# Kernel optimization log

Hardware: AMD Instinct MI355X
Metric: run time of the kernel (lower is better)

The kernel has to match this reference:

```python
import jax, jax.numpy as jnp
import numpy as np

NUM_HEADS = 32
HEAD_DIM = 128
NUM_KV_HEADS = 8
SCALE = 0.08838834764831845  # 1/sqrt(128)
T = 2048          # total packed tokens (total_q == total_k in delta branch)
N_SAL = 512       # number of salient rows
NUM_SEQS = 4
EPS = 1e-8
NEG = -1e30


def setup_inputs() -> dict:
    key = jax.random.key(0)
    ks = jax.random.split(key, 5)
    q = jax.random.normal(ks[0], (T, NUM_HEADS, HEAD_DIM), dtype=jnp.float32)
    k = jax.random.normal(ks[1], (T, NUM_KV_HEADS, HEAD_DIM), dtype=jnp.float32)
    v = jax.random.normal(ks[2], (N_SAL, NUM_KV_HEADS, HEAD_DIM), dtype=jnp.float32)
    v_cache = jax.random.normal(ks[3], (T, NUM_KV_HEADS, HEAD_DIM), dtype=jnp.float32)
    c_cache = jax.random.normal(ks[4], (T, NUM_HEADS * HEAD_DIM), dtype=jnp.float32)
    # unique, sorted salient row indices (torch index_copy requires well-defined scatter)
    idx_salient_row = (jnp.arange(N_SAL, dtype=jnp.int64) * (T // N_SAL))
    # 4 equal packed sequences
    cu_seqlens = jnp.array([0, 512, 1024, 1536, 2048], dtype=jnp.int64)
    return {"q": q, "k": k, "v": v, "v_cache": v_cache, "c_cache": c_cache,
            "idx_salient_row": idx_salient_row, "cu_seqlens": cu_seqlens}


def _segment_ids(cu_seqlens, n):
    # seg[i] = which packed sequence row i belongs to (searchsorted right on bounds)
    return jnp.searchsorted(cu_seqlens[1:], jnp.arange(n), side="right")


def _sdpa(q_, k_, v_, seg_q_, seg_k_):
    # GQA: repeat_interleave kv heads to match query heads
    n_rep = q_.shape[1] // k_.shape[1]
    if n_rep > 1:
        k_ = jnp.repeat(k_, n_rep, axis=1)
        v_ = jnp.repeat(v_, n_rep, axis=1)
    scores = jnp.einsum("qhd,khd->hqk", q_, k_) * SCALE  # [H, nq, T]
    allow = (seg_q_[:, None] == seg_k_[None, :])          # [nq, T]
    scores = jnp.where(allow[None, :, :], scores, NEG)
    p = jax.nn.softmax(scores, axis=-1)
    return jnp.einsum("hqk,khd->qhd", p, v_)              # [nq, H, D]


def reference(q, k, v, v_cache, c_cache, idx_salient_row, cu_seqlens):
    total = q.shape[0]
    seg = _segment_ids(cu_seqlens, total)  # seg_q == seg_k (total_q == total_k)

    # delta KV-cache update at salient rows
    v_delta = v - v_cache[idx_salient_row]                      # [n_sal, Hkv, D]
    v_delta_sparse = jnp.zeros_like(k).at[idx_salient_row].set(v_delta)
    v_cache_new = v_cache.at[idx_salient_row].set(v)

    # salient-row full attention against updated cache
    o_salient = _sdpa(q[idx_salient_row], k, v_cache_new, seg[idx_salient_row], seg)
    # sparse delta attention for every row
    delta_c = _sdpa(q, k, v_delta_sparse, seg, seg)

    new_c_flat = c_cache + delta_c.reshape(total, -1)
    new_c_flat = new_c_flat.at[idx_salient_row].set(o_salient.reshape(o_salient.shape[0], -1))

    # cosine similarity between old and new context (early-exit signal)
    num = jnp.sum(c_cache * new_c_flat, axis=-1)
    den_c = jnp.sum(c_cache * c_cache, axis=-1)
    den_n = jnp.sum(new_c_flat * new_c_flat, axis=-1)
    cos_sim = num / (jnp.sqrt(den_c) * jnp.sqrt(den_n) + EPS)

    return new_c_flat.reshape(total, NUM_HEADS, HEAD_DIM), cos_sim
```

## Files before the change

kernel.cpp:

```cpp
#include <hip/hip_runtime.h>
#include <math.h>

#define NUM_HEADS 32
#define HEAD_DIM 128
#define NUM_KV_HEADS 8
#define SCALE 0.08838834764831845f
#define EPS 1e-8f
#define MAX_SEG 512
#define QT 32
#define BLK 512
#define SEGC_MAX 16
#define PD_CHUNKS 4
#define SAL_PAD 576
#define PB_STRIDE 520
#define PD_STRIDE 136
#define TLD 130
#define CD (NUM_HEADS * HEAD_DIM)

typedef __bf16 bf16x8 __attribute__((ext_vector_type(8)));
typedef __bf16 bf16x4 __attribute__((ext_vector_type(4)));
typedef float  f32x4  __attribute__((ext_vector_type(4)));

__device__ __forceinline__ int lower_bound_i(const int* __restrict__ a, int n, int key) {
    int lo = 0, hi = n;
    while (lo < hi) { int mid = (lo + hi) >> 1; if (a[mid] < key) lo = mid + 1; else hi = mid; }
    return lo;
}
__device__ __forceinline__ int bsearch_eq(const int* __restrict__ a, int n, int key) {
    int lo = lower_bound_i(a, n, key);
    return (lo < n && a[lo] == key) ? lo : -1;
}

__global__ void prep(const float* __restrict__ k, const float* __restrict__ v,
                     const float* __restrict__ vc, const int* __restrict__ idx,
                     __bf16* __restrict__ kb, __bf16* __restrict__ vnewT,
                     __bf16* __restrict__ vdT, int T, int Tpad, int n_sal,
                     int nb_conv, int nb_vt) {
    __shared__ __bf16 tile[64 * TLD];
    __shared__ int sal_of[64];
    const int b = blockIdx.x;
    const int tid = threadIdx.x;

    if (b < nb_conv) {
        int i = b * 256 + tid;
        int n8 = T * NUM_KV_HEADS * HEAD_DIM / 8;
        if (i < n8) {
            const float4* s4 = (const float4*)(k + (size_t)i * 8);
            float4 a = s4[0], bb = s4[1];
            bf16x8 o;
            o[0]=(__bf16)a.x; o[1]=(__bf16)a.y; o[2]=(__bf16)a.z; o[3]=(__bf16)a.w;
            o[4]=(__bf16)bb.x; o[5]=(__bf16)bb.y; o[6]=(__bf16)bb.z; o[7]=(__bf16)bb.w;
            *(bf16x8*)(kb + (size_t)i * 8) = o;
        }
        return;
    }
    if (b < nb_conv + nb_vt * NUM_KV_HEADS) {
        const int bb = b - nb_conv;
        const int kv = bb / nb_vt;
        const int r0 = (bb % nb_vt) * 64;
        if (tid < 64) sal_of[tid] = bsearch_eq(idx, n_sal, r0 + tid);
        __syncthreads();
        for (int ii = tid; ii < 64 * 32; ii += 256) {
            int r = ii >> 5, c4 = ii & 31;
            int row = r0 + r;
            float4 f = {0.f, 0.f, 0.f, 0.f};
            if (row < T) {
                int s2 = sal_of[r];
                const float* src = (s2 >= 0)
                    ? v  + ((size_t)s2  * NUM_KV_HEADS + kv) * HEAD_DIM
                    : vc + ((size_t)row * NUM_KV_HEADS + kv) * HEAD_DIM;
                f = *(const float4*)(src + c4 * 4);
            }
            __bf16* tp = &tile[r * TLD + c4 * 4];
            tp[0] = (__bf16)f.x; tp[1] = (__bf16)f.y; tp[2] = (__bf16)f.z; tp[3] = (__bf16)f.w;
        }
        __syncthreads();
        for (int ii = tid; ii < 128 * 8; ii += 256) {
            int d = ii >> 3, rg = ii & 7;
            int row_out = r0 + rg * 8;
            if (row_out < Tpad) {
                bf16x8 o;
#pragma unroll
                for (int j = 0; j < 8; j++) o[j] = tile[(rg * 8 + j) * TLD + d];
                *(bf16x8*)(vnewT + ((size_t)kv * HEAD_DIM + d) * Tpad + row_out) = o;
            }
        }
        return;
    }
    {
        const int bb = b - nb_conv - nb_vt * NUM_KV_HEADS;
        const int nvd = SAL_PAD / 64;
        const int kv = bb / nvd;
        const int s0 = (bb % nvd) * 64;
        for (int ii = tid; ii < 64 * 32; ii += 256) {
            int r = ii >> 5, c4 = ii & 31;
            int s = s0 + r;
            float4 f = {0.f, 0.f, 0.f, 0.f};
            if (s < n_sal) {
                int row = idx[s];
                float4 a = *(const float4*)(v  + ((size_t)s   * NUM_KV_HEADS + kv) * HEAD_DIM + c4 * 4);
                float4 bb2 = *(const float4*)(vc + ((size_t)row * NUM_KV_HEADS + kv) * HEAD_DIM + c4 * 4);
                f.x = a.x - bb2.x; f.y = a.y - bb2.y; f.z = a.z - bb2.z; f.w = a.w - bb2.w;
            }
            __bf16* tp = &tile[r * TLD + c4 * 4];
            tp[0] = (__bf16)f.x; tp[1] = (__bf16)f.y; tp[2] = (__bf16)f.z; tp[3] = (__bf16)f.w;
        }
        __syncthreads();
        for (int ii = tid; ii < 128 * 8; ii += 256) {
            int d = ii >> 3, rg = ii & 7;
            bf16x8 o;
#pragma unroll
            for (int j = 0; j < 8; j++) o[j] = tile[(rg * 8 + j) * TLD + d];
            *(bf16x8*)(vdT + ((size_t)kv * HEAD_DIM + d) * SAL_PAD + s0 + rg * 8) = o;
        }
    }
}

__global__ __launch_bounds__(BLK, 4)
void attn_mfma(const float* __restrict__ q, const __bf16* __restrict__ kb,
               const __bf16* __restrict__ vnewT, const __bf16* __restrict__ vdT,
               const float* __restrict__ c_cache, const int* __restrict__ cu,
               const int* __restrict__ idx, float* __restrict__ out_c,
               float* __restrict__ cospart, int T, int Tpad, int n_seq, int n_sal) {
    const int qt    = blockIdx.x;
    const int h     = blockIdx.y;
    const int kvh   = h >> 2;
    const int qrow0 = qt * QT;
    const int tid   = threadIdx.x;
    const int wave  = tid >> 6;
    const int lane  = tid & 63;
    const int lm    = lane & 15;
    const int quad  = lane >> 4;

    __shared__ __align__(16) __bf16 Pb[QT * PB_STRIDE];
    __shared__ __align__(16) __bf16 Pd[QT * PD_STRIDE];
    __shared__ int   scol[MAX_SEG];
    __shared__ float wred[8 * QT];
    __shared__ float linv[QT];
    __shared__ int   salrow[QT];

    int seg_start = 0, seg_end = T;
    for (int s = 0; s < n_seq; s++) {
        int a = cu[s], bnd = cu[s + 1];
        if (qrow0 >= a && qrow0 < bnd) { seg_start = a; seg_end = bnd; }
    }
    const int seg_len = seg_end - seg_start;
    const int s_lo = lower_bound_i(idx, n_sal, seg_start);
    const int s_hi = lower_bound_i(idx, n_sal, seg_end);
    const int nss  = s_hi - s_lo;
    const int ntiles = (seg_len + 15) >> 4;
    const int SEGC   = (seg_len + 31) >> 5;

    const int dim = wave * 16 + lm;

    const float* cbase = c_cache + (size_t)qrow0 * CD + h * HEAD_DIM + dim;
    float cold[2][4];
#pragma unroll
    for (int rt = 0; rt < 2; rt++)
#pragma unroll
        for (int r = 0; r < 4; r++)
            cold[rt][r] = cbase[(size_t)(rt * 16 + quad * 4 + r) * CD];

    if (tid < QT) salrow[tid] = bsearch_eq(idx, n_sal, qrow0 + tid);
    for (int s = tid; s < nss; s += BLK) scol[s] = idx[s_lo + s] - seg_start;
    if (ntiles * 16 < SEGC * 32) {
        for (int ii = tid; ii < QT * 16; ii += BLK) {
            int row = ii >> 4, col = ntiles * 16 + (ii & 15);
            Pb[row * PB_STRIDE + col] = (__bf16)0.f;
        }
    }

    bf16x8 aq[2][4];
#pragma unroll
    for (int rt = 0; rt < 2; rt++) {
        const float* qp = q + ((size_t)(qrow0 + rt * 16 + lm) * NUM_HEADS + h) * HEAD_DIM + quad * 8;
#pragma unroll
        for (int cc = 0; cc < 4; cc++) {
            float4 f0 = *(const float4*)(qp + cc * 32);
            float4 f1 = *(const float4*)(qp + cc * 32 + 4);
            bf16x8 a;
            a[0]=(__bf16)f0.x; a[1]=(__bf16)f0.y; a[2]=(__bf16)f0.z; a[3]=(__bf16)f0.w;
            a[4]=(__bf16)f1.x; a[5]=(__bf16)f1.y; a[6]=(__bf16)f1.z; a[7]=(__bf16)f1.w;
            aq[rt][cc] = a;
        }
    }

    float ps[2] = {0.f, 0.f};
#pragma unroll
    for (int tt = 0; tt < 4; tt++) {
        const int t = wave * 4 + tt;
        if (t < ntiles) {
            int key = seg_start + t * 16 + lm;
            if (key >= seg_start + seg_len) key = seg_start + seg_len - 1;
            const __bf16* kp = kb + ((size_t)key * NUM_KV_HEADS + kvh) * HEAD_DIM + quad * 8;
            bf16x8 bk[4];
#pragma unroll
            for (int cc = 0; cc < 4; cc++) bk[cc] = *(const bf16x8*)(kp + cc * 32);
            f32x4 acc[2] = {{0.f,0.f,0.f,0.f},{0.f,0.f,0.f,0.f}};
#pragma unroll
            for (int cc = 0; cc < 4; cc++) {
                acc[0] = __builtin_amdgcn_mfma_f32_16x16x32_bf16(bk[cc], aq[0][cc], acc[0], 0, 0, 0);
                acc[1] = __builtin_amdgcn_mfma_f32_16x16x32_bf16(bk[cc], aq[1][cc], acc[1], 0, 0, 0);
            }
#pragma unroll
            for (int rt = 0; rt < 2; rt++) {
                bf16x4 pk;
#pragma unroll
                for (int r = 0; r < 4; r++) {
                    const int kl = t * 16 + quad * 4 + r;
                    float e = (kl < seg_len) ? __expf(acc[rt][r] * SCALE) : 0.f;
                    ps[rt] += e;
                    pk[r] = (__bf16)e;
                }
                *(bf16x4*)&Pb[(rt * 16 + lm) * PB_STRIDE + t * 16 + quad * 4] = pk;
            }
        }
    }
#pragma unroll
    for (int m = 16; m <= 32; m <<= 1) {
        ps[0] += __shfl_xor(ps[0], m, 64);
        ps[1] += __shfl_xor(ps[1], m, 64);
    }
    if (quad == 0) {
        wred[wave * QT + lm]      = ps[0];
        wred[wave * QT + 16 + lm] = ps[1];
    }
    __syncthreads();
    if (tid < QT) {
        float s = 0.f;
#pragma unroll
        for (int w = 0; w < 8; w++) s += wred[w * QT + tid];
        linv[tid] = 1.f / s;
    }

    f32x4 acc0a = {0.f,0.f,0.f,0.f}, acc0b = {0.f,0.f,0.f,0.f};
    f32x4 acc1a = {0.f,0.f,0.f,0.f}, acc1b = {0.f,0.f,0.f,0.f};
    const __bf16* vbase = vnewT + ((size_t)kvh * HEAD_DIM + dim) * Tpad + seg_start + quad * 8;
    const __bf16* pb0 = &Pb[lm * PB_STRIDE + quad * 8];
    const __bf16* pb1 = &Pb[(16 + lm) * PB_STRIDE + quad * 8];

#define PV_BODY(cc)  {                                                              \
        bf16x8 a0 = *(const bf16x8*)(pb0 + (cc) * 32);                              \
        bf16x8 a1 = *(const bf16x8*)(pb1 + (cc) * 32);                              \
        bf16x8 bv = *(const bf16x8*)(vbase + (cc) * 32);                            \
        if ((cc) & 1) {                                                             \
            acc0b = __builtin_amdgcn_mfma_f32_16x16x32_bf16(a0, bv, acc0b, 0, 0, 0);\
            acc1b = __builtin_amdgcn_mfma_f32_16x16x32_bf16(a1, bv, acc1b, 0, 0, 0);\
        } else {                                                                    \
            acc0a = __builtin_amdgcn_mfma_f32_16x16x32_bf16(a0, bv, acc0a, 0, 0, 0);\
            acc1a = __builtin_amdgcn_mfma_f32_16x16x32_bf16(a1, bv, acc1a, 0, 0, 0);\
        } }

    if (SEGC == SEGC_MAX) {
#pragma unroll
        for (int cc = 0; cc < SEGC_MAX; cc++) PV_BODY(cc)
    } else {
        for (int cc = 0; cc < SEGC; cc++) PV_BODY(cc)
    }
    f32x4 accF[2];
    accF[0] = acc0a + acc0b;
    accF[1] = acc1a + acc1b;

    f32x4 accD[2] = {{0.f,0.f,0.f,0.f},{0.f,0.f,0.f,0.f}};
    const int ndc = (nss + 31) >> 5;
    const bool al8 = ((s_lo & 7) == 0);
    const __bf16* vdbase = vdT + ((size_t)kvh * HEAD_DIM + dim) * SAL_PAD + s_lo + quad * 8;
    for (int base = 0; base < ndc; base += PD_CHUNKS) {
        const int bc = min(PD_CHUNKS, ndc - base);
        __syncthreads();
        for (int ii = tid; ii < QT * PD_CHUNKS * 32; ii += BLK) {
            int row = ii >> 7, srel = ii & 127;
            int s = base * 32 + srel;
            __bf16 e = (__bf16)0.f;
            if (srel < bc * 32 && s < nss) e = Pb[row * PB_STRIDE + scol[s]];
            Pd[row * PD_STRIDE + srel] = e;
        }
        __syncthreads();
#pragma unroll
        for (int dc = 0; dc < PD_CHUNKS; dc++) {
            if (dc < bc) {
                bf16x8 a0 = *(const bf16x8*)&Pd[lm * PD_STRIDE + dc * 32 + quad * 8];
                bf16x8 a1 = *(const bf16x8*)&Pd[(16 + lm) * PD_STRIDE + dc * 32 + quad * 8];
                const __bf16* vp = vdbase + (base + dc) * 32;
                bf16x8 bv;
                if (al8) bv = *(const bf16x8*)vp;
                else {
#pragma unroll
                    for (int j = 0; j < 8; j++) bv[j] = vp[j];
                }
                accD[0] = __builtin_amdgcn_mfma_f32_16x16x32_bf16(a0, bv, accD[0], 0, 0, 0);
                accD[1] = __builtin_amdgcn_mfma_f32_16x16x32_bf16(a1, bv, accD[1], 0, 0, 0);
            }
        }
    }
    __syncthreads();

    float* cp = (float*)Pd;
    float* obase = out_c + (size_t)qrow0 * CD + h * HEAD_DIM + dim;
#pragma unroll
    for (int rt = 0; rt < 2; rt++) {
#pragma unroll
        for (int r = 0; r < 4; r++) {
            const int row = rt * 16 + quad * 4 + r;
            const float c_old = cold[rt][r];
            const float li = linv[row];
            float o;
            if (salrow[row] >= 0) o = accF[rt][r] * li;
            else                  o = c_old + accD[rt][r] * li;
            obase[(size_t)row * CD] = o;
            float xn = o * c_old, xc = c_old * c_old, xd = o * o;
#pragma unroll
            for (int m = 1; m <= 8; m <<= 1) {
                xn += __shfl_xor(xn, m, 64);
                xc += __shfl_xor(xc, m, 64);
                xd += __shfl_xor(xd, m, 64);
            }
            if (lm == 0) {
                cp[(wave * 3 + 0) * QT + row] = xn;
                cp[(wave * 3 + 1) * QT + row] = xc;
                cp[(wave * 3 + 2) * QT + row] = xd;
            }
        }
    }
    __syncthreads();
    for (int ii = tid; ii < 3 * QT; ii += BLK) {
        int c = ii >> 5, row = ii & 31;
        float s = 0.f;
#pragma unroll
        for (int w = 0; w < 8; w++) s += cp[(w * 3 + c) * QT + row];
        cospart[((size_t)(qrow0 + row) * NUM_HEADS + h) * 3 + c] = s;
    }
}

__global__ void cos_finalize(const float* __restrict__ cospart, float* __restrict__ out_cos, int T) {
    int i = blockIdx.x * blockDim.x + threadIdx.x;
    if (i < T) {
        const float* p = cospart + (size_t)i * NUM_HEADS * 3;
        float n = 0.f, c = 0.f, d = 0.f;
#pragma unroll
        for (int h2 = 0; h2 < NUM_HEADS; h2++) {
            n += p[h2 * 3 + 0]; c += p[h2 * 3 + 1]; d += p[h2 * 3 + 2];
        }
        out_cos[i] = n / (sqrtf(c) * sqrtf(d) + EPS);
    }
}

extern "C" void kernel_launch(void* const* d_in, const int* in_sizes, int n_in,
                              void* d_out, int out_size, void* d_ws, size_t ws_size,
                              hipStream_t stream) {
    const float* q       = (const float*)d_in[0];
    const float* k       = (const float*)d_in[1];
    const float* v       = (const float*)d_in[2];
    const float* v_cache = (const float*)d_in[3];
    const float* c_cache = (const float*)d_in[4];
    const int*   idx     = (const int*)d_in[5];
    const int*   cu      = (const int*)d_in[6];

    const int T     = in_sizes[0] / CD;
    const int n_sal = in_sizes[5];
    const int n_seq = in_sizes[6] - 1;
    const int Tpad  = T + 32;

    float* out_c   = (float*)d_out;
    float* out_cos = out_c + (size_t)T * CD;

    char* wsp = (char*)d_ws;
    size_t off = 0;
    __bf16* kb = (__bf16*)(wsp + off);
    off += (((size_t)T * NUM_KV_HEADS * HEAD_DIM * 2) + 255) & ~(size_t)255;
    __bf16* vnewT = (__bf16*)(wsp + off);
    off += (((size_t)NUM_KV_HEADS * HEAD_DIM * Tpad * 2) + 255) & ~(size_t)255;
    __bf16* vdT = (__bf16*)(wsp + off);
    off += ((size_t)NUM_KV_HEADS * HEAD_DIM * SAL_PAD * 2 + 255) & ~(size_t)255;
    float* cospart = (float*)(wsp + off);
    off += ((size_t)T * NUM_HEADS * 3 * 4 + 255) & ~(size_t)255;
    (void)ws_size;

    const int nb_conv = (T * NUM_KV_HEADS * HEAD_DIM / 8 + 255) / 256;
    const int nb_vt   = (Tpad + 63) / 64;
    const int nb_vd   = SAL_PAD / 64;
    const int nb_tot  = nb_conv + nb_vt * NUM_KV_HEADS + nb_vd * NUM_KV_HEADS;

    prep<<<nb_tot, 256, 0, stream>>>(k, v, v_cache, idx, kb, vnewT, vdT,
                                     T, Tpad, n_sal, nb_conv, nb_vt);

    dim3 grid(T / QT, NUM_HEADS);
    attn_mfma<<<grid, BLK, 0, stream>>>(q, kb, vnewT, vdT, c_cache, cu, idx,
                                        out_c, cospart, T, Tpad, n_seq, n_sal);

    cos_finalize<<<(T + 255) / 256, 256, 0, stream>>>(cospart, out_cos, T);
}
```

Measured before the change: 240.9 us.

## Prefetch K, V and delta-V into registers and merge PV with delta MFMA loop

```diff
diff --git a/kernel.cpp b/kernel.cpp
--- a/kernel.cpp
+++ b/kernel.cpp
@@ -150,16 +150,15 @@
     const int nss  = s_hi - s_lo;
     const int ntiles = (seg_len + 15) >> 4;
     const int SEGC   = (seg_len + 31) >> 5;
+    const int ndc    = (nss + 31) >> 5;
+    const bool al8   = ((s_lo & 7) == 0);
+    const bool fast  = (SEGC == SEGC_MAX) && (ndc <= PD_CHUNKS);
 
     const int dim = wave * 16 + lm;
-
-    const float* cbase = c_cache + (size_t)qrow0 * CD + h * HEAD_DIM + dim;
-    float cold[2][4];
-#pragma unroll
-    for (int rt = 0; rt < 2; rt++)
-#pragma unroll
-        for (int r = 0; r < 4; r++)
-            cold[rt][r] = cbase[(size_t)(rt * 16 + quad * 4 + r) * CD];
+    const __bf16* vbase  = vnewT + ((size_t)kvh * HEAD_DIM + dim) * Tpad + seg_start + quad * 8;
+    const __bf16* vdbase = vdT + ((size_t)kvh * HEAD_DIM + dim) * SAL_PAD + s_lo + quad * 8;
+    const __bf16* pb0 = &Pb[lm * PB_STRIDE + quad * 8];
+    const __bf16* pb1 = &Pb[(16 + lm) * PB_STRIDE + quad * 8];
 
     if (tid < QT) salrow[tid] = bsearch_eq(idx, n_sal, qrow0 + tid);
     for (int s = tid; s < nss; s += BLK) scol[s] = idx[s_lo + s] - seg_start;
@@ -185,7 +184,7 @@
         }
     }
 
-    float ps[2] = {0.f, 0.f};
+    bf16x8 bk[4][4];
 #pragma unroll
     for (int tt = 0; tt < 4; tt++) {
         const int t = wave * 4 + tt;
@@ -193,14 +192,21 @@
             int key = seg_start + t * 16 + lm;
             if (key >= seg_start + seg_len) key = seg_start + seg_len - 1;
             const __bf16* kp = kb + ((size_t)key * NUM_KV_HEADS + kvh) * HEAD_DIM + quad * 8;
-            bf16x8 bk[4];
-#pragma unroll
-            for (int cc = 0; cc < 4; cc++) bk[cc] = *(const bf16x8*)(kp + cc * 32);
+#pragma unroll
+            for (int cc = 0; cc < 4; cc++) bk[tt][cc] = *(const bf16x8*)(kp + cc * 32);
+        }
+    }
+
+    float ps[2] = {0.f, 0.f};
+#pragma unroll
+    for (int tt = 0; tt < 4; tt++) {
+        const int t = wave * 4 + tt;
+        if (t < ntiles) {
             f32x4 acc[2] = {{0.f,0.f,0.f,0.f},{0.f,0.f,0.f,0.f}};
 #pragma unroll
             for (int cc = 0; cc < 4; cc++) {
-                acc[0] = __builtin_amdgcn_mfma_f32_16x16x32_bf16(bk[cc], aq[0][cc], acc[0], 0, 0, 0);
-                acc[1] = __builtin_amdgcn_mfma_f32_16x16x32_bf16(bk[cc], aq[1][cc], acc[1], 0, 0, 0);
+                acc[0] = __builtin_amdgcn_mfma_f32_16x16x32_bf16(bk[tt][cc], aq[0][cc], acc[0], 0, 0, 0);
+                acc[1] = __builtin_amdgcn_mfma_f32_16x16x32_bf16(bk[tt][cc], aq[1][cc], acc[1], 0, 0, 0);
             }
 #pragma unroll
             for (int rt = 0; rt < 2; rt++) {
@@ -225,75 +231,109 @@
         wred[wave * QT + lm]      = ps[0];
         wred[wave * QT + 16 + lm] = ps[1];
     }
-    __syncthreads();
-    if (tid < QT) {
-        float s = 0.f;
-#pragma unroll
-        for (int w = 0; w < 8; w++) s += wred[w * QT + tid];
-        linv[tid] = 1.f / s;
-    }
-
-    f32x4 acc0a = {0.f,0.f,0.f,0.f}, acc0b = {0.f,0.f,0.f,0.f};
-    f32x4 acc1a = {0.f,0.f,0.f,0.f}, acc1b = {0.f,0.f,0.f,0.f};
-    const __bf16* vbase = vnewT + ((size_t)kvh * HEAD_DIM + dim) * Tpad + seg_start + quad * 8;
-    const __bf16* pb0 = &Pb[lm * PB_STRIDE + quad * 8];
-    const __bf16* pb1 = &Pb[(16 + lm) * PB_STRIDE + quad * 8];
-
-#define PV_BODY(cc)  {                                                              \
-        bf16x8 a0 = *(const bf16x8*)(pb0 + (cc) * 32);                              \
-        bf16x8 a1 = *(const bf16x8*)(pb1 + (cc) * 32);                              \
-        bf16x8 bv = *(const bf16x8*)(vbase + (cc) * 32);                            \
-        if ((cc) & 1) {                                                             \
-            acc0b = __builtin_amdgcn_mfma_f32_16x16x32_bf16(a0, bv, acc0b, 0, 0, 0);\
-            acc1b = __builtin_amdgcn_mfma_f32_16x16x32_bf16(a1, bv, acc1b, 0, 0, 0);\
-        } else {                                                                    \
-            acc0a = __builtin_amdgcn_mfma_f32_16x16x32_bf16(a0, bv, acc0a, 0, 0, 0);\
-            acc1a = __builtin_amdgcn_mfma_f32_16x16x32_bf16(a1, bv, acc1a, 0, 0, 0);\
-        } }
-
-    if (SEGC == SEGC_MAX) {
-#pragma unroll
-        for (int cc = 0; cc < SEGC_MAX; cc++) PV_BODY(cc)
-    } else {
-        for (int cc = 0; cc < SEGC; cc++) PV_BODY(cc)
-    }
-    f32x4 accF[2];
-    accF[0] = acc0a + acc0b;
-    accF[1] = acc1a + acc1b;
-
+
+    const float* cbase = c_cache + (size_t)qrow0 * CD + h * HEAD_DIM + dim;
+    float cold[2][4];
+#pragma unroll
+    for (int rt = 0; rt < 2; rt++)
+#pragma unroll
+        for (int r = 0; r < 4; r++)
+            cold[rt][r] = cbase[(size_t)(rt * 16 + quad * 4 + r) * CD];
+
+    f32x4 accF[2] = {{0.f,0.f,0.f,0.f},{0.f,0.f,0.f,0.f}};
     f32x4 accD[2] = {{0.f,0.f,0.f,0.f},{0.f,0.f,0.f,0.f}};
-    const int ndc = (nss + 31) >> 5;
-    const bool al8 = ((s_lo & 7) == 0);
-    const __bf16* vdbase = vdT + ((size_t)kvh * HEAD_DIM + dim) * SAL_PAD + s_lo + quad * 8;
-    for (int base = 0; base < ndc; base += PD_CHUNKS) {
-        const int bc = min(PD_CHUNKS, ndc - base);
-        __syncthreads();
+
+    if (fast) {
+        bf16x8 vreg[SEGC_MAX];
+#pragma unroll
+        for (int cc = 0; cc < SEGC_MAX; cc++) vreg[cc] = *(const bf16x8*)(vbase + cc * 32);
+        bf16x8 vdreg[PD_CHUNKS];
+#pragma unroll
+        for (int dc = 0; dc < PD_CHUNKS; dc++) {
+            if (dc < ndc) {
+                const __bf16* vp = vdbase + dc * 32;
+                if (al8) vdreg[dc] = *(const bf16x8*)vp;
+                else {
+#pragma unroll
+                    for (int j = 0; j < 8; j++) vdreg[dc][j] = vp[j];
+                }
+            }
+        }
+        __syncthreads();
+        if (tid < QT) {
+            float s = 0.f;
+#pragma unroll
+            for (int w = 0; w < 8; w++) s += wred[w * QT + tid];
+            linv[tid] = 1.f / s;
+        }
         for (int ii = tid; ii < QT * PD_CHUNKS * 32; ii += BLK) {
             int row = ii >> 7, srel = ii & 127;
-            int s = base * 32 + srel;
             __bf16 e = (__bf16)0.f;
-            if (srel < bc * 32 && s < nss) e = Pb[row * PB_STRIDE + scol[s]];
+            if (srel < nss) e = Pb[row * PB_STRIDE + scol[srel]];
             Pd[row * PD_STRIDE + srel] = e;
         }
         __syncthreads();
 #pragma unroll
-        for (int dc = 0; dc < PD_CHUNKS; dc++) {
-            if (dc < bc) {
-                bf16x8 a0 = *(const bf16x8*)&Pd[lm * PD_STRIDE + dc * 32 + quad * 8];
-                bf16x8 a1 = *(const bf16x8*)&Pd[(16 + lm) * PD_STRIDE + dc * 32 + quad * 8];
-                const __bf16* vp = vdbase + (base + dc) * 32;
-                bf16x8 bv;
-                if (al8) bv = *(const bf16x8*)vp;
-                else {
-#pragma unroll
-                    for (int j = 0; j < 8; j++) bv[j] = vp[j];
+        for (int cc = 0; cc < SEGC_MAX; cc++) {
+            bf16x8 a0 = *(const bf16x8*)(pb0 + cc * 32);
+            bf16x8 a1 = *(const bf16x8*)(pb1 + cc * 32);
+            accF[0] = __builtin_amdgcn_mfma_f32_16x16x32_bf16(a0, vreg[cc], accF[0], 0, 0, 0);
+            accF[1] = __builtin_amdgcn_mfma_f32_16x16x32_bf16(a1, vreg[cc], accF[1], 0, 0, 0);
+            if (cc < PD_CHUNKS) {
+                if (cc * 32 < nss) {
+                    bf16x8 d0 = *(const bf16x8*)&Pd[lm * PD_STRIDE + cc * 32 + quad * 8];
+                    bf16x8 d1 = *(const bf16x8*)&Pd[(16 + lm) * PD_STRIDE + cc * 32 + quad * 8];
+                    accD[0] = __builtin_amdgcn_mfma_f32_16x16x32_bf16(d0, vdreg[cc], accD[0], 0, 0, 0);
+                    accD[1] = __builtin_amdgcn_mfma_f32_16x16x32_bf16(d1, vdreg[cc], accD[1], 0, 0, 0);
                 }
-                accD[0] = __builtin_amdgcn_mfma_f32_16x16x32_bf16(a0, bv, accD[0], 0, 0, 0);
-                accD[1] = __builtin_amdgcn_mfma_f32_16x16x32_bf16(a1, bv, accD[1], 0, 0, 0);
-            }
-        }
-    }
-    __syncthreads();
+            }
+        }
+        __syncthreads();
+    } else {
+        __syncthreads();
+        if (tid < QT) {
+            float s = 0.f;
+#pragma unroll
+            for (int w = 0; w < 8; w++) s += wred[w * QT + tid];
+            linv[tid] = 1.f / s;
+        }
+        for (int cc = 0; cc < SEGC; cc++) {
+            bf16x8 a0 = *(const bf16x8*)(pb0 + cc * 32);
+            bf16x8 a1 = *(const bf16x8*)(pb1 + cc * 32);
+            bf16x8 bv = *(const bf16x8*)(vbase + cc * 32);
+            accF[0] = __builtin_amdgcn_mfma_f32_16x16x32_bf16(a0, bv, accF[0], 0, 0, 0);
+            accF[1] = __builtin_amdgcn_mfma_f32_16x16x32_bf16(a1, bv, accF[1], 0, 0, 0);
+        }
+        for (int base = 0; base < ndc; base += PD_CHUNKS) {
+            const int bc = min(PD_CHUNKS, ndc - base);
+            __syncthreads();
+            for (int ii = tid; ii < QT * PD_CHUNKS * 32; ii += BLK) {
+                int row = ii >> 7, srel = ii & 127;
+                int s = base * 32 + srel;
+                __bf16 e = (__bf16)0.f;
+                if (srel < bc * 32 && s < nss) e = Pb[row * PB_STRIDE + scol[s]];
+                Pd[row * PD_STRIDE + srel] = e;
+            }
+            __syncthreads();
+#pragma unroll
+            for (int dc = 0; dc < PD_CHUNKS; dc++) {
+                if (dc < bc) {
+                    bf16x8 d0 = *(const bf16x8*)&Pd[lm * PD_STRIDE + dc * 32 + quad * 8];
+                    bf16x8 d1 = *(const bf16x8*)&Pd[(16 + lm) * PD_STRIDE + dc * 32 + quad * 8];
+                    const __bf16* vp = vdbase + (base + dc) * 32;
+                    bf16x8 bv;
+                    if (al8) bv = *(const bf16x8*)vp;
+                    else {
+#pragma unroll
+                        for (int j = 0; j < 8; j++) bv[j] = vp[j];
+                    }
+                    accD[0] = __builtin_amdgcn_mfma_f32_16x16x32_bf16(d0, bv, accD[0], 0, 0, 0);
+                    accD[1] = __builtin_amdgcn_mfma_f32_16x16x32_bf16(d1, bv, accD[1], 0, 0, 0);
+                }
+            }
+        }
+        __syncthreads();
+    }
 
     float* cp = (float*)Pd;
     float* obase = out_c + (size_t)qrow0 * CD + h * HEAD_DIM + dim;
```

After: 256.3 us. 6.4% more time.

## Halve query tile to 16 rows and fuse cosine finalize via atomics

Applied to the files above, without the earlier changes.

```diff
diff --git a/kernel.cpp b/kernel.cpp
--- a/kernel.cpp
+++ b/kernel.cpp
@@ -7,8 +7,8 @@
 #define SCALE 0.08838834764831845f
 #define EPS 1e-8f
 #define MAX_SEG 512
-#define QT 32
-#define BLK 512
+#define QT 16
+#define BLK 256
 #define SEGC_MAX 16
 #define PD_CHUNKS 4
 #define SAL_PAD 576
@@ -34,15 +34,21 @@
 __global__ void prep(const float* __restrict__ k, const float* __restrict__ v,
                      const float* __restrict__ vc, const int* __restrict__ idx,
                      __bf16* __restrict__ kb, __bf16* __restrict__ vnewT,
-                     __bf16* __restrict__ vdT, int T, int Tpad, int n_sal,
-                     int nb_conv, int nb_vt) {
+                     __bf16* __restrict__ vdT, int* __restrict__ zbase,
+                     int T, int Tpad, int n_sal,
+                     int nb_zero, int nb_conv, int nb_vt) {
     __shared__ __bf16 tile[64 * TLD];
     __shared__ int sal_of[64];
     const int b = blockIdx.x;
     const int tid = threadIdx.x;
 
-    if (b < nb_conv) {
+    if (b < nb_zero) {
         int i = b * 256 + tid;
+        if (i < T * 4) zbase[i] = 0;
+        return;
+    }
+    if (b < nb_zero + nb_conv) {
+        int i = (b - nb_zero) * 256 + tid;
         int n8 = T * NUM_KV_HEADS * HEAD_DIM / 8;
         if (i < n8) {
             const float4* s4 = (const float4*)(k + (size_t)i * 8);
@@ -54,8 +60,8 @@
         }
         return;
     }
-    if (b < nb_conv + nb_vt * NUM_KV_HEADS) {
-        const int bb = b - nb_conv;
+    if (b < nb_zero + nb_conv + nb_vt * NUM_KV_HEADS) {
+        const int bb = b - nb_zero - nb_conv;
         const int kv = bb / nb_vt;
         const int r0 = (bb % nb_vt) * 64;
         if (tid < 64) sal_of[tid] = bsearch_eq(idx, n_sal, r0 + tid);
@@ -88,7 +94,7 @@
         return;
     }
     {
-        const int bb = b - nb_conv - nb_vt * NUM_KV_HEADS;
+        const int bb = b - nb_zero - nb_conv - nb_vt * NUM_KV_HEADS;
         const int nvd = SAL_PAD / 64;
         const int kv = bb / nvd;
         const int s0 = (bb % nvd) * 64;
@@ -121,7 +127,8 @@
                const __bf16* __restrict__ vnewT, const __bf16* __restrict__ vdT,
                const float* __restrict__ c_cache, const int* __restrict__ cu,
                const int* __restrict__ idx, float* __restrict__ out_c,
-               float* __restrict__ cospart, int T, int Tpad, int n_seq, int n_sal) {
+               float* __restrict__ cospart, int* __restrict__ cnt,
+               float* __restrict__ out_cos, int T, int Tpad, int n_seq, int n_sal) {
     const int qt    = blockIdx.x;
     const int h     = blockIdx.y;
     const int kvh   = h >> 2;
@@ -135,7 +142,7 @@
     __shared__ __align__(16) __bf16 Pb[QT * PB_STRIDE];
     __shared__ __align__(16) __bf16 Pd[QT * PD_STRIDE];
     __shared__ int   scol[MAX_SEG];
-    __shared__ float wred[8 * QT];
+    __shared__ float wred[4 * QT];
     __shared__ float linv[QT];
     __shared__ int   salrow[QT];
 
@@ -150,16 +157,8 @@
     const int nss  = s_hi - s_lo;
     const int ntiles = (seg_len + 15) >> 4;
     const int SEGC   = (seg_len + 31) >> 5;
-
-    const int dim = wave * 16 + lm;
-
-    const float* cbase = c_cache + (size_t)qrow0 * CD + h * HEAD_DIM + dim;
-    float cold[2][4];
-#pragma unroll
-    for (int rt = 0; rt < 2; rt++)
-#pragma unroll
-        for (int r = 0; r < 4; r++)
-            cold[rt][r] = cbase[(size_t)(rt * 16 + quad * 4 + r) * CD];
+    const int ndc    = (nss + 31) >> 5;
+    const bool al8   = ((s_lo & 7) == 0);
 
     if (tid < QT) salrow[tid] = bsearch_eq(idx, n_sal, qrow0 + tid);
     for (int s = tid; s < nss; s += BLK) scol[s] = idx[s_lo + s] - seg_start;
@@ -170,10 +169,9 @@
         }
     }
 
-    bf16x8 aq[2][4];
-#pragma unroll
-    for (int rt = 0; rt < 2; rt++) {
-        const float* qp = q + ((size_t)(qrow0 + rt * 16 + lm) * NUM_HEADS + h) * HEAD_DIM + quad * 8;
+    bf16x8 aq[4];
+    {
+        const float* qp = q + ((size_t)(qrow0 + lm) * NUM_HEADS + h) * HEAD_DIM + quad * 8;
 #pragma unroll
         for (int cc = 0; cc < 4; cc++) {
             float4 f0 = *(const float4*)(qp + cc * 32);
@@ -181,93 +179,76 @@
             bf16x8 a;
             a[0]=(__bf16)f0.x; a[1]=(__bf16)f0.y; a[2]=(__bf16)f0.z; a[3]=(__bf16)f0.w;
             a[4]=(__bf16)f1.x; a[5]=(__bf16)f1.y; a[6]=(__bf16)f1.z; a[7]=(__bf16)f1.w;
-            aq[rt][cc] = a;
-        }
-    }
-
-    float ps[2] = {0.f, 0.f};
-#pragma unroll
-    for (int tt = 0; tt < 4; tt++) {
-        const int t = wave * 4 + tt;
+            aq[cc] = a;
+        }
+    }
+
+    float ps = 0.f;
+#pragma unroll
+    for (int tt = 0; tt < 8; tt++) {
+        const int t = wave * 8 + tt;
         if (t < ntiles) {
             int key = seg_start + t * 16 + lm;
             if (key >= seg_start + seg_len) key = seg_start + seg_len - 1;
             const __bf16* kp = kb + ((size_t)key * NUM_KV_HEADS + kvh) * HEAD_DIM + quad * 8;
-            bf16x8 bk[4];
-#pragma unroll
-            for (int cc = 0; cc < 4; cc++) bk[cc] = *(const bf16x8*)(kp + cc * 32);
-            f32x4 acc[2] = {{0.f,0.f,0.f,0.f},{0.f,0.f,0.f,0.f}};
+            f32x4 acc = {0.f, 0.f, 0.f, 0.f};
 #pragma unroll
             for (int cc = 0; cc < 4; cc++) {
-                acc[0] = __builtin_amdgcn_mfma_f32_16x16x32_bf16(bk[cc], aq[0][cc], acc[0], 0, 0, 0);
-                acc[1] = __builtin_amdgcn_mfma_f32_16x16x32_bf16(bk[cc], aq[1][cc], acc[1], 0, 0, 0);
-            }
-#pragma unroll
-            for (int rt = 0; rt < 2; rt++) {
-                bf16x4 pk;
-#pragma unroll
-                for (int r = 0; r < 4; r++) {
-                    const int kl = t * 16 + quad * 4 + r;
-                    float e = (kl < seg_len) ? __expf(acc[rt][r] * SCALE) : 0.f;
-                    ps[rt] += e;
-                    pk[r] = (__bf16)e;
-                }
-                *(bf16x4*)&Pb[(rt * 16 + lm) * PB_STRIDE + t * 16 + quad * 4] = pk;
-            }
-        }
-    }
-#pragma unroll
-    for (int m = 16; m <= 32; m <<= 1) {
-        ps[0] += __shfl_xor(ps[0], m, 64);
-        ps[1] += __shfl_xor(ps[1], m, 64);
-    }
-    if (quad == 0) {
-        wred[wave * QT + lm]      = ps[0];
-        wred[wave * QT + 16 + lm] = ps[1];
-    }
+                bf16x8 bk = *(const bf16x8*)(kp + cc * 32);
+                acc = __builtin_amdgcn_mfma_f32_16x16x32_bf16(bk, aq[cc], acc, 0, 0, 0);
+            }
+            bf16x4 pk;
+#pragma unroll
+            for (int r = 0; r < 4; r++) {
+                const int kl = t * 16 + quad * 4 + r;
+                float e = (kl < seg_len) ? __expf(acc[r] * SCALE) : 0.f;
+                ps += e;
+                pk[r] = (__bf16)e;
+            }
+            *(bf16x4*)&Pb[lm * PB_STRIDE + t * 16 + quad * 4] = pk;
+        }
+    }
+#pragma unroll
+    for (int m = 16; m <= 32; m <<= 1) ps += __shfl_xor(ps, m, 64);
+    if (quad == 0) wred[wave * QT + lm] = ps;
+
+    float cold[2][4];
+#pragma unroll
+    for (int nt = 0; nt < 2; nt++) {
+        const int dim = nt * 64 + wave * 16 + lm;
+        const float* cbase = c_cache + (size_t)qrow0 * CD + h * HEAD_DIM + dim;
+#pragma unroll
+        for (int r = 0; r < 4; r++)
+            cold[nt][r] = cbase[(size_t)(quad * 4 + r) * CD];
+    }
+
     __syncthreads();
     if (tid < QT) {
         float s = 0.f;
 #pragma unroll
-        for (int w = 0; w < 8; w++) s += wred[w * QT + tid];
+        for (int w = 0; w < 4; w++) s += wred[w * QT + tid];
         linv[tid] = 1.f / s;
     }
 
-    f32x4 acc0a = {0.f,0.f,0.f,0.f}, acc0b = {0.f,0.f,0.f,0.f};
-    f32x4 acc1a = {0.f,0.f,0.f,0.f}, acc1b = {0.f,0.f,0.f,0.f};
-    const __bf16* vbase = vnewT + ((size_t)kvh * HEAD_DIM + dim) * Tpad + seg_start + quad * 8;
-    const __bf16* pb0 = &Pb[lm * PB_STRIDE + quad * 8];
-    const __bf16* pb1 = &Pb[(16 + lm) * PB_STRIDE + quad * 8];
-
-#define PV_BODY(cc)  {                                                              \
-        bf16x8 a0 = *(const bf16x8*)(pb0 + (cc) * 32);                              \
-        bf16x8 a1 = *(const bf16x8*)(pb1 + (cc) * 32);                              \
-        bf16x8 bv = *(const bf16x8*)(vbase + (cc) * 32);                            \
-        if ((cc) & 1) {                                                             \
-            acc0b = __builtin_amdgcn_mfma_f32_16x16x32_bf16(a0, bv, acc0b, 0, 0, 0);\
-            acc1b = __builtin_amdgcn_mfma_f32_16x16x32_bf16(a1, bv, acc1b, 0, 0, 0);\
-        } else {                                                                    \
-            acc0a = __builtin_amdgcn_mfma_f32_16x16x32_bf16(a0, bv, acc0a, 0, 0, 0);\
-            acc1a = __builtin_amdgcn_mfma_f32_16x16x32_bf16(a1, bv, acc1a, 0, 0, 0);\
-        } }
-
-    if (SEGC == SEGC_MAX) {
-#pragma unroll
-        for (int cc = 0; cc < SEGC_MAX; cc++) PV_BODY(cc)
-    } else {
-        for (int cc = 0; cc < SEGC; cc++) PV_BODY(cc)
-    }
-    f32x4 accF[2];
-    accF[0] = acc0a + acc0b;
-    accF[1] = acc1a + acc1b;
-
+    f32x4 accF[2] = {{0.f,0.f,0.f,0.f},{0.f,0.f,0.f,0.f}};
     f32x4 accD[2] = {{0.f,0.f,0.f,0.f},{0.f,0.f,0.f,0.f}};
-    const int ndc = (nss + 31) >> 5;
-    const bool al8 = ((s_lo & 7) == 0);
-    const __bf16* vdbase = vdT + ((size_t)kvh * HEAD_DIM + dim) * SAL_PAD + s_lo + quad * 8;
+    const __bf16* vb0 = vnewT + ((size_t)kvh * HEAD_DIM + wave * 16 + lm) * Tpad + seg_start + quad * 8;
+    const __bf16* vb1 = vnewT + ((size_t)kvh * HEAD_DIM + 64 + wave * 16 + lm) * Tpad + seg_start + quad * 8;
+    const __bf16* pbp = &Pb[lm * PB_STRIDE + quad * 8];
+#pragma unroll 2
+    for (int cc = 0; cc < SEGC; cc++) {
+        bf16x8 a  = *(const bf16x8*)(pbp + cc * 32);
+        bf16x8 v0 = *(const bf16x8*)(vb0 + cc * 32);
+        bf16x8 v1 = *(const bf16x8*)(vb1 + cc * 32);
+        accF[0] = __builtin_amdgcn_mfma_f32_16x16x32_bf16(a, v0, accF[0], 0, 0, 0);
+        accF[1] = __builtin_amdgcn_mfma_f32_16x16x32_bf16(a, v1, accF[1], 0, 0, 0);
+    }
+
+    const __bf16* vd0 = vdT + ((size_t)kvh * HEAD_DIM + wave * 16 + lm) * SAL_PAD + s_lo + quad * 8;
+    const __bf16* vd1 = vdT + ((size_t)kvh * HEAD_DIM + 64 + wave * 16 + lm) * SAL_PAD + s_lo + quad * 8;
     for (int base = 0; base < ndc; base += PD_CHUNKS) {
         const int bc = min(PD_CHUNKS, ndc - base);
-        __syncthreads();
+        if (base > 0) __syncthreads();
         for (int ii = tid; ii < QT * PD_CHUNKS * 32; ii += BLK) {
             int row = ii >> 7, srel = ii & 127;
             int s = base * 32 + srel;
@@ -279,69 +260,78 @@
 #pragma unroll
         for (int dc = 0; dc < PD_CHUNKS; dc++) {
             if (dc < bc) {
-                bf16x8 a0 = *(const bf16x8*)&Pd[lm * PD_STRIDE + dc * 32 + quad * 8];
-                bf16x8 a1 = *(const bf16x8*)&Pd[(16 + lm) * PD_STRIDE + dc * 32 + quad * 8];
-                const __bf16* vp = vdbase + (base + dc) * 32;
-                bf16x8 bv;
-                if (al8) bv = *(const bf16x8*)vp;
+                bf16x8 a = *(const bf16x8*)&Pd[lm * PD_STRIDE + dc * 32 + quad * 8];
+                const __bf16 *p0 = vd0 + (base + dc) * 32, *p1 = vd1 + (base + dc) * 32;
+                bf16x8 w0, w1;
+                if (al8) { w0 = *(const bf16x8*)p0; w1 = *(const bf16x8*)p1; }
                 else {
 #pragma unroll
-                    for (int j = 0; j < 8; j++) bv[j] = vp[j];
+                    for (int j = 0; j < 8; j++) { w0[j] = p0[j]; w1[j] = p1[j]; }
                 }
-                accD[0] = __builtin_amdgcn_mfma_f32_16x16x32_bf16(a0, bv, accD[0], 0, 0, 0);
-                accD[1] = __builtin_amdgcn_mfma_f32_16x16x32_bf16(a1, bv, accD[1], 0, 0, 0);
+                accD[0] = __builtin_amdgcn_mfma_f32_16x16x32_bf16(a, w0, accD[0], 0, 0, 0);
+                accD[1] = __builtin_amdgcn_mfma_f32_16x16x32_bf16(a, w1, accD[1], 0, 0, 0);
             }
         }
     }
     __syncthreads();
 
     float* cp = (float*)Pd;
-    float* obase = out_c + (size_t)qrow0 * CD + h * HEAD_DIM + dim;
-#pragma unroll
-    for (int rt = 0; rt < 2; rt++) {
+    float xn[4], xc[4], xd[4];
+#pragma unroll
+    for (int r = 0; r < 4; r++) { xn[r] = 0.f; xc[r] = 0.f; xd[r] = 0.f; }
+#pragma unroll
+    for (int nt = 0; nt < 2; nt++) {
+        const int dim = nt * 64 + wave * 16 + lm;
+        float* obase = out_c + (size_t)qrow0 * CD + h * HEAD_DIM + dim;
 #pragma unroll
         for (int r = 0; r < 4; r++) {
-            const int row = rt * 16 + quad * 4 + r;
-            const float c_old = cold[rt][r];
+            const int row = quad * 4 + r;
+            const float c_old = cold[nt][r];
             const float li = linv[row];
             float o;
-            if (salrow[row] >= 0) o = accF[rt][r] * li;
-            else                  o = c_old + accD[rt][r] * li;
+            if (salrow[row] >= 0) o = accF[nt][r] * li;
+            else                  o = c_old + accD[nt][r] * li;
             obase[(size_t)row * CD] = o;
-            float xn = o * c_old, xc = c_old * c_old, xd = o * o;
-#pragma unroll
-            for (int m = 1; m <= 8; m <<= 1) {
-                xn += __shfl_xor(xn, m, 64);
-                xc += __shfl_xor(xc, m, 64);
-                xd += __shfl_xor(xd, m, 64);
-            }
-            if (lm == 0) {
-                cp[(wave * 3 + 0) * QT + row] = xn;
-                cp[(wave * 3 + 1) * QT + row] = xc;
-                cp[(wave * 3 + 2) * QT + row] = xd;
-            }
+            xn[r] += o * c_old; xc[r] += c_old * c_old; xd[r] += o * o;
+        }
+    }
+#pragma unroll
+    for (int r = 0; r < 4; r++) {
+#pragma unroll
+        for (int m = 1; m <= 8; m <<= 1) {
+            xn[r] += __shfl_xor(xn[r], m, 64);
+            xc[r] += __shfl_xor(xc[r], m, 64);
+            xd[r] += __shfl_xor(xd[r], m, 64);
+        }
+        if (lm == 0) {
+            const int row = quad * 4 + r;
+            cp[(wave * 3 + 0) * QT + row] = xn[r];
+            cp[(wave * 3 + 1) * QT + row] = xc[r];
+            cp[(wave * 3 + 2) * QT + row] = xd[r];
         }
     }
     __syncthreads();
-    for (int ii = tid; ii < 3 * QT; ii += BLK) {
-        int c = ii >> 5, row = ii & 31;
-        float s = 0.f;
-#pragma unroll
-        for (int w = 0; w < 8; w++) s += cp[(w * 3 + c) * QT + row];
-        cospart[((size_t)(qrow0 + row) * NUM_HEADS + h) * 3 + c] = s;
-    }
-}
-
-__global__ void cos_finalize(const float* __restrict__ cospart, float* __restrict__ out_cos, int T) {
-    int i = blockIdx.x * blockDim.x + threadIdx.x;
-    if (i < T) {
-        const float* p = cospart + (size_t)i * NUM_HEADS * 3;
+    if (tid < QT) {
+        const int rg = qrow0 + tid;
         float n = 0.f, c = 0.f, d = 0.f;
 #pragma unroll
-        for (int h2 = 0; h2 < NUM_HEADS; h2++) {
-            n += p[h2 * 3 + 0]; c += p[h2 * 3 + 1]; d += p[h2 * 3 + 2];
-        }
-        out_cos[i] = n / (sqrtf(c) * sqrtf(d) + EPS);
+        for (int w = 0; w < 4; w++) {
+            n += cp[(w * 3 + 0) * QT + tid];
+            c += cp[(w * 3 + 1) * QT + tid];
+            d += cp[(w * 3 + 2) * QT + tid];
+        }
+        atomicAdd(&cospart[rg * 3 + 0], n);
+        atomicAdd(&cospart[rg * 3 + 1], c);
+        atomicAdd(&cospart[rg * 3 + 2], d);
+        __threadfence();
+        int old = atomicAdd(&cnt[rg], 1);
+        if (old == NUM_HEADS - 1) {
+            __threadfence();
+            float fn = atomicAdd(&cospart[rg * 3 + 0], 0.f);
+            float fc = atomicAdd(&cospart[rg * 3 + 1], 0.f);
+            float fd = atomicAdd(&cospart[rg * 3 + 2], 0.f);
+            out_cos[rg] = fn / (sqrtf(fc) * sqrtf(fd) + EPS);
+        }
     }
 }
 
@@ -373,20 +363,22 @@
     __bf16* vdT = (__bf16*)(wsp + off);
     off += ((size_t)NUM_KV_HEADS * HEAD_DIM * SAL_PAD * 2 + 255) & ~(size_t)255;
     float* cospart = (float*)(wsp + off);
-    off += ((size_t)T * NUM_HEADS * 3 * 4 + 255) & ~(size_t)255;
+    int*   cnt     = (int*)(cospart + (size_t)T * 3);
+    off += ((size_t)T * 4 * 4 + 255) & ~(size_t)255;
     (void)ws_size;
 
+    const int nb_zero = (T * 4 + 255) / 256;
     const int nb_conv = (T * NUM_KV_HEADS * HEAD_DIM / 8 + 255) / 256;
     const int nb_vt   = (Tpad + 63) / 64;
     const int nb_vd   = SAL_PAD / 64;
-    const int nb_tot  = nb_conv + nb_vt * NUM_KV_HEADS + nb_vd * NUM_KV_HEADS;
+    const int nb_tot  = nb_zero + nb_conv + nb_vt * NUM_KV_HEADS + nb_vd * NUM_KV_HEADS;
 
     prep<<<nb_tot, 256, 0, stream>>>(k, v, v_cache, idx, kb, vnewT, vdT,
-                                     T, Tpad, n_sal, nb_conv, nb_vt);
+                                     (int*)cospart, T, Tpad, n_sal,
+                                     nb_zero, nb_conv, nb_vt);
 
     dim3 grid(T / QT, NUM_HEADS);
     attn_mfma<<<grid, BLK, 0, stream>>>(q, kb, vnewT, vdT, c_cache, cu, idx,
-                                        out_c, cospart, T, Tpad, n_seq, n_sal);
-
-    cos_finalize<<<(T + 255) / 256, 256, 0, stream>>>(cospart, out_cos, T);
-}
+                                        out_c, cospart, cnt, out_cos,
+                                        T, Tpad, n_seq, n_sal);
+}
```

New measurement: 413.5 us. 1.72x slower.
